# Kernel tuning notes

Measured on AMD Instinct MI355X. Metric: run time of the kernel, lower is better.

Reference implementation:

```python
import jax, jax.numpy as jnp
import numpy as np

VOCAB, EMB, HID, B, T = 50000, 16, 32, 4096, 500


def setup_inputs() -> dict:
    key = jax.random.key(0)
    k1, k2, k3, k4 = jax.random.split(key, 4)
    tokens = jax.random.randint(k1, (B, T), 0, VOCAB, dtype=jnp.int32)
    emb_table = jax.random.normal(k2, (VOCAB, EMB), dtype=jnp.float32) * 0.05
    kernel = jax.random.normal(k3, (EMB, 4 * HID), dtype=jnp.float32) * (1.0 / np.sqrt(EMB))
    rec_kernel = jax.random.normal(k4, (HID, 4 * HID), dtype=jnp.float32) * (1.0 / np.sqrt(HID))
    # Keras default: unit_forget_bias=True -> forget-gate bias = 1
    bias = jnp.concatenate([
        jnp.zeros((HID,), jnp.float32),
        jnp.ones((HID,), jnp.float32),
        jnp.zeros((2 * HID,), jnp.float32),
    ])
    return {"tokens": tokens, "emb_table": emb_table, "kernel": kernel,
            "rec_kernel": rec_kernel, "bias": bias}


def reference(tokens, emb_table, kernel, rec_kernel, bias):
    # Embedding with mask_zero=True: mask = tokens != 0
    embedded = emb_table[tokens]                 # [B, T, EMB]
    mask = (tokens != 0)                         # [B, T] bool
    # Precompute input projections for all timesteps (one big GEMM)
    x_proj = jnp.einsum('bte,eh->bth', embedded, kernel) + bias  # [B, T, 4H]

    def step(carry, xs):
        h, c = carry                              # [B, H] each
        xp_t, m_t = xs                            # [B, 4H], [B]
        z = xp_t + h @ rec_kernel                 # [B, 4H]
        i, f, g, o = jnp.split(z, 4, axis=-1)     # Keras gate order i,f,c,o
        i = jax.nn.sigmoid(i)
        f = jax.nn.sigmoid(f)
        g = jnp.tanh(g)
        o = jax.nn.sigmoid(o)
        c_new = f * c + i * g
        h_new = o * jnp.tanh(c_new)
        m = m_t[:, None]
        # masked steps carry previous state through (Keras LSTM mask semantics)
        h = jnp.where(m, h_new, h)
        c = jnp.where(m, c_new, c)
        return (h, c), None

    h0 = jnp.zeros((tokens.shape[0], HID), jnp.float32)
    c0 = jnp.zeros((tokens.shape[0], HID), jnp.float32)
    xs = (jnp.swapaxes(x_proj, 0, 1), jnp.swapaxes(mask, 0, 1))  # time-major
    (h, c), _ = jax.lax.scan(step, (h0, c0), xs)
    return h                                      # [B, HID] last (masked) output
```

## Files before the change

kernel.cpp:

```cpp
#include <hip/hip_runtime.h>
#include <cstdint>

#define VOCAB_N 50000
#define EMB_N   16
#define HID_N   32
#define B_N     4096
#define T_N     500
#define LOG2E     1.4426950408889634f
#define TWOLOG2E  2.8853900817779268f

typedef __attribute__((ext_vector_type(8))) short bf16x8;
typedef __attribute__((ext_vector_type(4))) float f32x4;
typedef __attribute__((ext_vector_type(4))) unsigned int u32x4;

__device__ __forceinline__ float frcp(float x) { return __builtin_amdgcn_rcpf(x); }

__device__ __forceinline__ unsigned bf16_split_pack(float x) {
  unsigned u  = __builtin_bit_cast(unsigned, x);
  float hif = __builtin_bit_cast(float, u & 0xFFFF0000u);
  float r   = x - hif;
  unsigned lo = __builtin_bit_cast(unsigned, r) >> 16;
  return (u >> 16) | (lo << 16);
}
__device__ __forceinline__ float unpack_h(unsigned p) {
  float hi = __builtin_bit_cast(float, p << 16);
  float lo = __builtin_bit_cast(float, p & 0xFFFF0000u);
  return hi + lo;
}

__global__ void build_proj_ns(const float* __restrict__ emb,
                              const float* __restrict__ W,
                              const float* __restrict__ bias,
                              float* __restrict__ proj) {
  __shared__ float Wl[EMB_N * 128];
  __shared__ float bl[128];
  const int tid = threadIdx.x;
  for (int i = tid; i < EMB_N * 128 / 4; i += 256)
    reinterpret_cast<float4*>(Wl)[i] = reinterpret_cast<const float4*>(W)[i];
  if (tid < 32)
    reinterpret_cast<float4*>(bl)[tid] = reinterpret_cast<const float4*>(bias)[tid];
  __syncthreads();

  const long long gid = (long long)blockIdx.x * 256 + tid;
  if (gid >= (long long)VOCAB_N * 128) return;
  const int v = (int)(gid >> 7);
  const int q = (int)(gid & 127);
  const int c  = q >> 3;
  const int par = (q >> 2) & 1;
  const int n2 = q & 3;
  const int col = (2 * n2 + par) * 16 + c;

  const float4* ev = reinterpret_cast<const float4*>(emb + (size_t)v * EMB_N);
  float4 e0 = ev[0], e1 = ev[1], e2 = ev[2], e3 = ev[3];
  const float em[16] = {e0.x,e0.y,e0.z,e0.w, e1.x,e1.y,e1.z,e1.w,
                        e2.x,e2.y,e2.z,e2.w, e3.x,e3.y,e3.z,e3.w};
  float a = bl[col];
#pragma unroll
  for (int e = 0; e < EMB_N; ++e) a = fmaf(em[e], Wl[e * 128 + col], a);
  proj[gid] = a * LOG2E;
}

#define GATE(R, TOK, CC, HH)                                                  \
  {                                                                           \
    float zi = z0[R], zf = z1[R], zg = z2[R], zo = z3[R];                     \
    float gi = frcp(1.0f + exp2f(-zi));                                       \
    float gf = frcp(1.0f + exp2f(-zf));                                       \
    float gg = fmaf(-2.0f, frcp(1.0f + exp2f(zg + zg)), 1.0f);                \
    float go = frcp(1.0f + exp2f(-zo));                                       \
    float cn = fmaf(gf, CC, gi * gg);                                         \
    float tc = fmaf(-2.0f, frcp(1.0f + exp2f(cn * TWOLOG2E)), 1.0f);          \
    float hn = go * tc;                                                       \
    bool m = (TOK) != 0;                                                      \
    CC = m ? cn : CC;                                                         \
    unsigned hp_ = bf16_split_pack(hn);                                       \
    HH = m ? hp_ : HH;                                                        \
    hl[pp ^ 1][rb + (R)][unit] = HH;                                          \
  }

#define BODY(TM, TP, X0, X1, X2, X3, TT4)                                     \
  {                                                                           \
    const unsigned* hrow = &hl[pp][c16][g8];                                  \
    u32x4 wa = *reinterpret_cast<const u32x4*>(hrow);                         \
    u32x4 wb = *reinterpret_cast<const u32x4*>(hrow + 4);                     \
    u32x4 ahp, alp;                                                           \
    ahp[0] = __builtin_amdgcn_perm(wa[1], wa[0], 0x05040100u);                \
    alp[0] = __builtin_amdgcn_perm(wa[1], wa[0], 0x07060302u);                \
    ahp[1] = __builtin_amdgcn_perm(wa[3], wa[2], 0x05040100u);                \
    alp[1] = __builtin_amdgcn_perm(wa[3], wa[2], 0x07060302u);                \
    ahp[2] = __builtin_amdgcn_perm(wb[1], wb[0], 0x05040100u);                \
    alp[2] = __builtin_amdgcn_perm(wb[1], wb[0], 0x07060302u);                \
    ahp[3] = __builtin_amdgcn_perm(wb[3], wb[2], 0x05040100u);                \
    alp[3] = __builtin_amdgcn_perm(wb[3], wb[2], 0x07060302u);                \
    bf16x8 Ah = __builtin_bit_cast(bf16x8, ahp);                              \
    bf16x8 Al = __builtin_bit_cast(bf16x8, alp);                              \
    f32x4 z0 = {(X0).x, (X1).x, (X2).x, (X3).x};                              \
    f32x4 z1 = {(X0).y, (X1).y, (X2).y, (X3).y};                              \
    f32x4 z2 = {(X0).z, (X1).z, (X2).z, (X3).z};                              \
    f32x4 z3 = {(X0).w, (X1).w, (X2).w, (X3).w};                              \
    \
    (X0) = *reinterpret_cast<const float4*>(projw + (size_t)(TP).x * 128);    \
    (X1) = *reinterpret_cast<const float4*>(projw + (size_t)(TP).y * 128);    \
    (X2) = *reinterpret_cast<const float4*>(projw + (size_t)(TP).z * 128);    \
    (X3) = *reinterpret_cast<const float4*>(projw + (size_t)(TP).w * 128);    \
    z0 = __builtin_amdgcn_mfma_f32_16x16x32_bf16(Ah, Bh0, z0, 0, 0, 0);       \
    z1 = __builtin_amdgcn_mfma_f32_16x16x32_bf16(Ah, Bh1, z1, 0, 0, 0);       \
    z2 = __builtin_amdgcn_mfma_f32_16x16x32_bf16(Ah, Bh2, z2, 0, 0, 0);       \
    z3 = __builtin_amdgcn_mfma_f32_16x16x32_bf16(Ah, Bh3, z3, 0, 0, 0);       \
    z0 = __builtin_amdgcn_mfma_f32_16x16x32_bf16(Al, Bh0, z0, 0, 0, 0);       \
    z1 = __builtin_amdgcn_mfma_f32_16x16x32_bf16(Al, Bh1, z1, 0, 0, 0);       \
    z2 = __builtin_amdgcn_mfma_f32_16x16x32_bf16(Al, Bh2, z2, 0, 0, 0);       \
    z3 = __builtin_amdgcn_mfma_f32_16x16x32_bf16(Al, Bh3, z3, 0, 0, 0);       \
    z0 = __builtin_amdgcn_mfma_f32_16x16x32_bf16(Ah, Bl0, z0, 0, 0, 0);       \
    z1 = __builtin_amdgcn_mfma_f32_16x16x32_bf16(Ah, Bl1, z1, 0, 0, 0);       \
    z2 = __builtin_amdgcn_mfma_f32_16x16x32_bf16(Ah, Bl2, z2, 0, 0, 0);       \
    z3 = __builtin_amdgcn_mfma_f32_16x16x32_bf16(Ah, Bl3, z3, 0, 0, 0);       \
                                                  \
    int4 tnew = make_int4(tokl[rb + 0][TT4], tokl[rb + 1][TT4],               \
                          tokl[rb + 2][TT4], tokl[rb + 3][TT4]);              \
    GATE(0, (TM).x, c0, hr0)                                                  \
    GATE(1, (TM).y, c1, hr1)                                                  \
    GATE(2, (TM).z, c2, hr2)                                                  \
    GATE(3, (TM).w, c3, hr3)                                                  \
    asm volatile("s_waitcnt lgkmcnt(0)" ::: "memory");                        \
    __builtin_amdgcn_s_barrier();                                             \
    asm volatile("" ::: "memory");                                            \
    __builtin_amdgcn_sched_barrier(0);                                        \
    pp ^= 1;                                                                  \
    (TM) = (TP); (TP) = tnew;                                                 \
  }

__global__ __launch_bounds__(128, 1)
void lstm_mfma_ns(const int*   __restrict__ tokens,
                  const float* __restrict__ rec_kernel,
                  const float* __restrict__ proj,
                  float*       __restrict__ out) {
  __shared__ int      tokl[16][512];
  __shared__ unsigned hl[2][16][36];

  const int tid = threadIdx.x;
  const int wv  = tid >> 6;
  const int l   = tid & 63;
  const int c16 = l & 15;
  const int g   = l >> 4;
  const int g8  = g * 8;
  const int rb  = g * 4;
  const int unit = wv * 16 + c16;

  {
    const int4* src = reinterpret_cast<const int4*>(tokens + (size_t)blockIdx.x * 16 * T_N);
    for (int i = tid; i < 16 * T_N / 4; i += 128) {
      int4 v4 = src[i];
      int gi = 4 * i;
      int r  = gi / T_N;
      int cc = gi - r * T_N;
      *reinterpret_cast<int4*>(&tokl[r][cc]) = v4;
    }
    for (int i = tid; i < 16 * 12; i += 128) {
      int r = i / 12; tokl[r][T_N + (i % 12)] = 0;
    }
  }

  hl[0][rb + 0][unit] = 0; hl[0][rb + 1][unit] = 0;
  hl[0][rb + 2][unit] = 0; hl[0][rb + 3][unit] = 0;

  bf16x8 Bh0, Bh1, Bh2, Bh3, Bl0, Bl1, Bl2, Bl3;
#define BUILD_B(Q, BH, BL)                                                    \
  {                                                                           \
    _Pragma("unroll")                                                         \
    for (int j = 0; j < 8; ++j) {                                             \
      float x = rec_kernel[(g8 + j) * 128 + (2 * (Q) + wv) * 16 + c16] * LOG2E;\
      unsigned s_ = bf16_split_pack(x);                                       \
      (BH)[j] = (short)s_; (BL)[j] = (short)(s_ >> 16);                       \
    }                                                                         \
  }
  BUILD_B(0, Bh0, Bl0) BUILD_B(1, Bh1, Bl1)
  BUILD_B(2, Bh2, Bl2) BUILD_B(3, Bh3, Bl3)
#undef BUILD_B

  __syncthreads();

  float    c0 = 0.f, c1 = 0.f, c2 = 0.f, c3 = 0.f;
  unsigned hr0 = 0, hr1 = 0, hr2 = 0, hr3 = 0;
  int pp = 0;

  int4 tmA = make_int4(tokl[rb+0][0], tokl[rb+1][0], tokl[rb+2][0], tokl[rb+3][0]);
  int4 tmB = make_int4(tokl[rb+0][1], tokl[rb+1][1], tokl[rb+2][1], tokl[rb+3][1]);
  int4 tpA = make_int4(tokl[rb+0][2], tokl[rb+1][2], tokl[rb+2][2], tokl[rb+3][2]);
  int4 tpB = make_int4(tokl[rb+0][3], tokl[rb+1][3], tokl[rb+2][3], tokl[rb+3][3]);

  const float* projw = proj + c16 * 8 + wv * 4;
  float4 xA0 = *reinterpret_cast<const float4*>(projw + (size_t)tmA.x * 128);
  float4 xA1 = *reinterpret_cast<const float4*>(projw + (size_t)tmA.y * 128);
  float4 xA2 = *reinterpret_cast<const float4*>(projw + (size_t)tmA.z * 128);
  float4 xA3 = *reinterpret_cast<const float4*>(projw + (size_t)tmA.w * 128);
  float4 xB0 = *reinterpret_cast<const float4*>(projw + (size_t)tmB.x * 128);
  float4 xB1 = *reinterpret_cast<const float4*>(projw + (size_t)tmB.y * 128);
  float4 xB2 = *reinterpret_cast<const float4*>(projw + (size_t)tmB.z * 128);
  float4 xB3 = *reinterpret_cast<const float4*>(projw + (size_t)tmB.w * 128);

#pragma unroll 1
  for (int t = 0; t < T_N; t += 2) {
    BODY(tmA, tpA, xA0, xA1, xA2, xA3, t + 4);
    BODY(tmB, tpB, xB0, xB1, xB2, xB3, t + 5);
  }

  const size_t obase = (size_t)blockIdx.x * 16 + rb;
  out[(obase + 0) * HID_N + unit] = unpack_h(hr0);
  out[(obase + 1) * HID_N + unit] = unpack_h(hr1);
  out[(obase + 2) * HID_N + unit] = unpack_h(hr2);
  out[(obase + 3) * HID_N + unit] = unpack_h(hr3);
}

__device__ __forceinline__ float sigm_fb(float x) {
  return frcp(1.0f + exp2f(x * -1.4426950408889634f));
}
__device__ __forceinline__ float tanh_fb(float x) {
  float e = exp2f(x * 2.8853900817779268f);
  return fmaf(-2.0f, frcp(e + 1.0f), 1.0f);
}

__global__ __launch_bounds__(256, 2)
void lstm_scan_fallback(const int*   __restrict__ tokens,
                        const float* __restrict__ rec_kernel,
                        const float* __restrict__ emb,
                        const float* __restrict__ W,
                        const float* __restrict__ bias,
                        float*       __restrict__ out) {
  __shared__ int   tokl[8][T_N];
  __shared__ float hbuf[8][HID_N];

  const int tid  = threadIdx.x;
  const int wv   = tid >> 6;
  const int lane = tid & 63;
  const int half = lane >> 5;
  const int j    = lane & 31;
  const int wrow = wv * 2 + half;
  const int row  = blockIdx.x * 8 + wrow;

  {
    const int4* src = reinterpret_cast<const int4*>(tokens + (size_t)blockIdx.x * 8 * T_N);
    int4* dst = reinterpret_cast<int4*>(&tokl[0][0]);
    for (int i = tid; i < 8 * T_N / 4; i += 256) dst[i] = src[i];
  }

  float wr[HID_N][4];
#pragma unroll
  for (int k = 0; k < HID_N; ++k)
#pragma unroll
    for (int gg2 = 0; gg2 < 4; ++gg2) wr[k][gg2] = rec_kernel[k * 128 + gg2 * 32 + j];

  float wk[EMB_N][4];
  float bb[4];
#pragma unroll
  for (int e = 0; e < EMB_N; ++e)
#pragma unroll
    for (int gg2 = 0; gg2 < 4; ++gg2) wk[e][gg2] = W[e * 128 + gg2 * 32 + j];
#pragma unroll
  for (int gg2 = 0; gg2 < 4; ++gg2) bb[gg2] = bias[gg2 * 32 + j];
  __syncthreads();

  float c = 0.0f, h = 0.0f;
  float4 h4[8];
#pragma unroll
  for (int q = 0; q < 8; ++q) h4[q] = make_float4(0.f, 0.f, 0.f, 0.f);

  for (int t = 0; t < T_N; ++t) {
    const int tokc = tokl[wrow][t];
    const float4* ev = reinterpret_cast<const float4*>(emb + (size_t)tokc * EMB_N);
    float4 e0 = ev[0], e1 = ev[1], e2 = ev[2], e3 = ev[3];
    const float em[16] = {e0.x,e0.y,e0.z,e0.w, e1.x,e1.y,e1.z,e1.w,
                          e2.x,e2.y,e2.z,e2.w, e3.x,e3.y,e3.z,e3.w};
    float a0 = bb[0], a1 = bb[1], a2 = bb[2], a3 = bb[3];
#pragma unroll
    for (int e = 0; e < EMB_N; ++e) {
      float x = em[e];
      a0 = fmaf(x, wk[e][0], a0); a1 = fmaf(x, wk[e][1], a1);
      a2 = fmaf(x, wk[e][2], a2); a3 = fmaf(x, wk[e][3], a3);
    }
#pragma unroll
    for (int q = 0; q < 8; ++q) {
      float hx = h4[q].x, hy = h4[q].y, hz = h4[q].z, hw = h4[q].w;
      a0 = fmaf(hx, wr[4*q+0][0], a0); a1 = fmaf(hx, wr[4*q+0][1], a1);
      a2 = fmaf(hx, wr[4*q+0][2], a2); a3 = fmaf(hx, wr[4*q+0][3], a3);
      a0 = fmaf(hy, wr[4*q+1][0], a0); a1 = fmaf(hy, wr[4*q+1][1], a1);
      a2 = fmaf(hy, wr[4*q+1][2], a2); a3 = fmaf(hy, wr[4*q+1][3], a3);
      a0 = fmaf(hz, wr[4*q+2][0], a0); a1 = fmaf(hz, wr[4*q+2][1], a1);
      a2 = fmaf(hz, wr[4*q+2][2], a2); a3 = fmaf(hz, wr[4*q+2][3], a3);
      a0 = fmaf(hw, wr[4*q+3][0], a0); a1 = fmaf(hw, wr[4*q+3][1], a1);
      a2 = fmaf(hw, wr[4*q+3][2], a2); a3 = fmaf(hw, wr[4*q+3][3], a3);
    }
    float ig = sigm_fb(a0), fg = sigm_fb(a1), gg = tanh_fb(a2), og = sigm_fb(a3);
    float cn = fmaf(fg, c, ig * gg);
    float hn = og * tanh_fb(cn);
    if (tokc != 0) { h = hn; c = cn; }
    hbuf[wrow][j] = h;
    asm volatile("" ::: "memory");
#pragma unroll
    for (int q = 0; q < 8; ++q)
      h4[q] = reinterpret_cast<const float4*>(&hbuf[wrow][0])[q];
    asm volatile("" ::: "memory");
  }
  out[(size_t)row * HID_N + j] = h;
}

extern "C" void kernel_launch(void* const* d_in, const int* in_sizes, int n_in,
                              void* d_out, int out_size, void* d_ws, size_t ws_size,
                              hipStream_t stream) {
  const int*   tokens = (const int*)  d_in[0];
  const float* emb    = (const float*)d_in[1];
  const float* W      = (const float*)d_in[2];
  const float* rec    = (const float*)d_in[3];
  const float* bias   = (const float*)d_in[4];
  float* out = (float*)d_out;

  const size_t need = (size_t)VOCAB_N * 128 * sizeof(float);
  if (ws_size >= need) {
    float* proj = (float*)d_ws;
    const long long total = (long long)VOCAB_N * 128;
    build_proj_ns<<<(int)((total + 255) / 256), 256, 0, stream>>>(emb, W, bias, proj);
    lstm_mfma_ns<<<B_N / 16, 128, 0, stream>>>(tokens, rec, proj, out);
  } else {
    lstm_scan_fallback<<<B_N / 8, 256, 0, stream>>>(tokens, rec, emb, W, bias, out);
  }
}
```

Before: 392.9 us.

## Transpose LSTM recurrence into single-wave MFMA with register-resident hidden state

The recurrent matmul is rewritten as W^T·h^T, so one 64-lane wave per 16-row batch tile holds all 128 gate columns. The hidden state stays in registers, packed as the MFMA B operand, which removes the per-step LDS round trip and the two-wave barrier. The projection table is permuted to match the new output layout, and the tanh-gate columns are prescaled by 2·log2e so the gate math saves a multiply. In exchange each wave issues 24 MFMAs per step with only 64 threads per block, which lowers occupancy and latency hiding.

After: 709.8 us. 1.81x slower.

```diff
diff --git a/kernel.cpp b/kernel.cpp
--- a/kernel.cpp
+++ b/kernel.cpp
@@ -28,10 +28,19 @@
   return hi + lo;
 }
 
-__global__ void build_proj_ns(const float* __restrict__ emb,
-                              const float* __restrict__ W,
-                              const float* __restrict__ bias,
-                              float* __restrict__ proj) {
+__device__ __forceinline__ int map_col(int p) {
+  int n = p >> 4, s = p & 15;
+  int g = s >> 2, r = s & 3;
+  return 32 * (n >> 1) + 8 * g + 2 * r + (n & 1);
+}
+__device__ __forceinline__ float col_scale(int n) {
+  return (n == 4 || n == 5) ? TWOLOG2E : LOG2E;
+}
+
+__global__ void build_proj_t(const float* __restrict__ emb,
+                             const float* __restrict__ W,
+                             const float* __restrict__ bias,
+                             float* __restrict__ proj) {
   __shared__ float Wl[EMB_N * 128];
   __shared__ float bl[128];
   const int tid = threadIdx.x;
@@ -44,11 +53,9 @@
   const long long gid = (long long)blockIdx.x * 256 + tid;
   if (gid >= (long long)VOCAB_N * 128) return;
   const int v = (int)(gid >> 7);
-  const int q = (int)(gid & 127);
-  const int c  = q >> 3;
-  const int par = (q >> 2) & 1;
-  const int n2 = q & 3;
-  const int col = (2 * n2 + par) * 16 + c;
+  const int p = (int)(gid & 127);
+  const int col = map_col(p);
+  const float sc = col_scale(p >> 4);
 
   const float4* ev = reinterpret_cast<const float4*>(emb + (size_t)v * EMB_N);
   float4 e0 = ev[0], e1 = ev[1], e2 = ev[2], e3 = ev[3];
@@ -57,158 +64,176 @@
   float a = bl[col];
 #pragma unroll
   for (int e = 0; e < EMB_N; ++e) a = fmaf(em[e], Wl[e * 128 + col], a);
-  proj[gid] = a * LOG2E;
-}
-
-#define GATE(R, TOK, CC, HH)                                                  \
+  proj[gid] = a * sc;
+}
+
+#define MF(A_, B_, C_) __builtin_amdgcn_mfma_f32_16x16x32_bf16((A_), (B_), (C_), 0, 0, 0)
+
+#define GATE(HP, CC, ZI, ZF, ZG, ZO, R)                                       \
   {                                                                           \
-    float zi = z0[R], zf = z1[R], zg = z2[R], zo = z3[R];                     \
+    float zi = (ZI)[R], zf = (ZF)[R], zg = (ZG)[R], zo = (ZO)[R];             \
     float gi = frcp(1.0f + exp2f(-zi));                                       \
     float gf = frcp(1.0f + exp2f(-zf));                                       \
-    float gg = fmaf(-2.0f, frcp(1.0f + exp2f(zg + zg)), 1.0f);                \
+    float gg = fmaf(-2.0f, frcp(1.0f + exp2f(zg)), 1.0f);                     \
     float go = frcp(1.0f + exp2f(-zo));                                       \
-    float cn = fmaf(gf, CC, gi * gg);                                         \
+    float cn = fmaf(gf, (CC), gi * gg);                                       \
     float tc = fmaf(-2.0f, frcp(1.0f + exp2f(cn * TWOLOG2E)), 1.0f);          \
     float hn = go * tc;                                                       \
-    bool m = (TOK) != 0;                                                      \
-    CC = m ? cn : CC;                                                         \
+    (CC) = mk ? cn : (CC);                                                    \
     unsigned hp_ = bf16_split_pack(hn);                                       \
-    HH = m ? hp_ : HH;                                                        \
-    hl[pp ^ 1][rb + (R)][unit] = HH;                                          \
-  }
-
-#define BODY(TM, TP, X0, X1, X2, X3, TT4)                                     \
+    (HP) = mk ? hp_ : (HP);                                                   \
+  }
+
+#define MBODY(TKC, TKP, XX0, XX1, XX2, XX3, XX4, XX5, XX6, XX7)               \
   {                                                                           \
-    const unsigned* hrow = &hl[pp][c16][g8];                                  \
-    u32x4 wa = *reinterpret_cast<const u32x4*>(hrow);                         \
-    u32x4 wb = *reinterpret_cast<const u32x4*>(hrow + 4);                     \
-    u32x4 ahp, alp;                                                           \
-    ahp[0] = __builtin_amdgcn_perm(wa[1], wa[0], 0x05040100u);                \
-    alp[0] = __builtin_amdgcn_perm(wa[1], wa[0], 0x07060302u);                \
-    ahp[1] = __builtin_amdgcn_perm(wa[3], wa[2], 0x05040100u);                \
-    alp[1] = __builtin_amdgcn_perm(wa[3], wa[2], 0x07060302u);                \
-    ahp[2] = __builtin_amdgcn_perm(wb[1], wb[0], 0x05040100u);                \
-    alp[2] = __builtin_amdgcn_perm(wb[1], wb[0], 0x07060302u);                \
-    ahp[3] = __builtin_amdgcn_perm(wb[3], wb[2], 0x05040100u);                \
-    alp[3] = __builtin_amdgcn_perm(wb[3], wb[2], 0x07060302u);                \
-    bf16x8 Ah = __builtin_bit_cast(bf16x8, ahp);                              \
-    bf16x8 Al = __builtin_bit_cast(bf16x8, alp);                              \
-    f32x4 z0 = {(X0).x, (X1).x, (X2).x, (X3).x};                              \
-    f32x4 z1 = {(X0).y, (X1).y, (X2).y, (X3).y};                              \
-    f32x4 z2 = {(X0).z, (X1).z, (X2).z, (X3).z};                              \
-    f32x4 z3 = {(X0).w, (X1).w, (X2).w, (X3).w};                              \
-    \
-    (X0) = *reinterpret_cast<const float4*>(projw + (size_t)(TP).x * 128);    \
-    (X1) = *reinterpret_cast<const float4*>(projw + (size_t)(TP).y * 128);    \
-    (X2) = *reinterpret_cast<const float4*>(projw + (size_t)(TP).z * 128);    \
-    (X3) = *reinterpret_cast<const float4*>(projw + (size_t)(TP).w * 128);    \
-    z0 = __builtin_amdgcn_mfma_f32_16x16x32_bf16(Ah, Bh0, z0, 0, 0, 0);       \
-    z1 = __builtin_amdgcn_mfma_f32_16x16x32_bf16(Ah, Bh1, z1, 0, 0, 0);       \
-    z2 = __builtin_amdgcn_mfma_f32_16x16x32_bf16(Ah, Bh2, z2, 0, 0, 0);       \
-    z3 = __builtin_amdgcn_mfma_f32_16x16x32_bf16(Ah, Bh3, z3, 0, 0, 0);       \
-    z0 = __builtin_amdgcn_mfma_f32_16x16x32_bf16(Al, Bh0, z0, 0, 0, 0);       \
-    z1 = __builtin_amdgcn_mfma_f32_16x16x32_bf16(Al, Bh1, z1, 0, 0, 0);       \
-    z2 = __builtin_amdgcn_mfma_f32_16x16x32_bf16(Al, Bh2, z2, 0, 0, 0);       \
-    z3 = __builtin_amdgcn_mfma_f32_16x16x32_bf16(Al, Bh3, z3, 0, 0, 0);       \
-    z0 = __builtin_amdgcn_mfma_f32_16x16x32_bf16(Ah, Bl0, z0, 0, 0, 0);       \
-    z1 = __builtin_amdgcn_mfma_f32_16x16x32_bf16(Ah, Bl1, z1, 0, 0, 0);       \
-    z2 = __builtin_amdgcn_mfma_f32_16x16x32_bf16(Ah, Bl2, z2, 0, 0, 0);       \
-    z3 = __builtin_amdgcn_mfma_f32_16x16x32_bf16(Ah, Bl3, z3, 0, 0, 0);       \
-                                                  \
-    int4 tnew = make_int4(tokl[rb + 0][TT4], tokl[rb + 1][TT4],               \
-                          tokl[rb + 2][TT4], tokl[rb + 3][TT4]);              \
-    GATE(0, (TM).x, c0, hr0)                                                  \
-    GATE(1, (TM).y, c1, hr1)                                                  \
-    GATE(2, (TM).z, c2, hr2)                                                  \
-    GATE(3, (TM).w, c3, hr3)                                                  \
-    asm volatile("s_waitcnt lgkmcnt(0)" ::: "memory");                        \
-    __builtin_amdgcn_s_barrier();                                             \
-    asm volatile("" ::: "memory");                                            \
-    __builtin_amdgcn_sched_barrier(0);                                        \
-    pp ^= 1;                                                                  \
-    (TM) = (TP); (TP) = tnew;                                                 \
-  }
-
-__global__ __launch_bounds__(128, 1)
-void lstm_mfma_ns(const int*   __restrict__ tokens,
-                  const float* __restrict__ rec_kernel,
-                  const float* __restrict__ proj,
-                  float*       __restrict__ out) {
-  __shared__ int      tokl[16][512];
-  __shared__ unsigned hl[2][16][36];
-
-  const int tid = threadIdx.x;
-  const int wv  = tid >> 6;
-  const int l   = tid & 63;
+                  \
+    u32x4 bhv, blv;                                                           \
+    bhv[0] = __builtin_amdgcn_perm(hp1, hp0, 0x05040100u);                    \
+    blv[0] = __builtin_amdgcn_perm(hp1, hp0, 0x07060302u);                    \
+    bhv[1] = __builtin_amdgcn_perm(hp3, hp2, 0x05040100u);                    \
+    blv[1] = __builtin_amdgcn_perm(hp3, hp2, 0x07060302u);                    \
+    bhv[2] = __builtin_amdgcn_perm(hp5, hp4, 0x05040100u);                    \
+    blv[2] = __builtin_amdgcn_perm(hp5, hp4, 0x07060302u);                    \
+    bhv[3] = __builtin_amdgcn_perm(hp7, hp6, 0x05040100u);                    \
+    blv[3] = __builtin_amdgcn_perm(hp7, hp6, 0x07060302u);                    \
+    bf16x8 Bh = __builtin_bit_cast(bf16x8, bhv);                              \
+    bf16x8 Bl = __builtin_bit_cast(bf16x8, blv);                              \
+    f32x4 za0 = __builtin_bit_cast(f32x4, XX0);                               \
+    f32x4 za1 = __builtin_bit_cast(f32x4, XX1);                               \
+    f32x4 za2 = __builtin_bit_cast(f32x4, XX2);                               \
+    f32x4 za3 = __builtin_bit_cast(f32x4, XX3);                               \
+    f32x4 za4 = __builtin_bit_cast(f32x4, XX4);                               \
+    f32x4 za5 = __builtin_bit_cast(f32x4, XX5);                               \
+    f32x4 za6 = __builtin_bit_cast(f32x4, XX6);                               \
+    f32x4 za7 = __builtin_bit_cast(f32x4, XX7);                               \
+                                     \
+    za0 = MF(Ah0, Bh, za0); za0 = MF(Ah0, Bl, za0); za0 = MF(Al0, Bh, za0);   \
+    za2 = MF(Ah2, Bh, za2); za2 = MF(Ah2, Bl, za2); za2 = MF(Al2, Bh, za2);   \
+    za4 = MF(Ah4, Bh, za4); za4 = MF(Ah4, Bl, za4); za4 = MF(Al4, Bh, za4);   \
+    za6 = MF(Ah6, Bh, za6); za6 = MF(Ah6, Bl, za6); za6 = MF(Al6, Bh, za6);   \
+                              \
+    {                                                                         \
+      const float* pv = proj + ((size_t)(unsigned)(TKP) << 7) + g4;           \
+      XX0 = *reinterpret_cast<const float4*>(pv);                             \
+      XX1 = *reinterpret_cast<const float4*>(pv + 16);                        \
+      XX2 = *reinterpret_cast<const float4*>(pv + 32);                        \
+      XX3 = *reinterpret_cast<const float4*>(pv + 48);                        \
+      XX4 = *reinterpret_cast<const float4*>(pv + 64);                        \
+      XX5 = *reinterpret_cast<const float4*>(pv + 80);                        \
+      XX6 = *reinterpret_cast<const float4*>(pv + 96);                        \
+      XX7 = *reinterpret_cast<const float4*>(pv + 112);                       \
+    }                                                                         \
+    const bool mk = (TKC) != 0;                                               \
+    GATE(hp0, cc0, za0, za2, za4, za6, 0)                                     \
+    GATE(hp2, cc2, za0, za2, za4, za6, 1)                                     \
+    GATE(hp4, cc4, za0, za2, za4, za6, 2)                                     \
+    GATE(hp6, cc6, za0, za2, za4, za6, 3)                                     \
+    za1 = MF(Ah1, Bh, za1); za1 = MF(Ah1, Bl, za1); za1 = MF(Al1, Bh, za1);   \
+    za3 = MF(Ah3, Bh, za3); za3 = MF(Ah3, Bl, za3); za3 = MF(Al3, Bh, za3);   \
+    za5 = MF(Ah5, Bh, za5); za5 = MF(Ah5, Bl, za5); za5 = MF(Al5, Bh, za5);   \
+    za7 = MF(Ah7, Bh, za7); za7 = MF(Ah7, Bl, za7); za7 = MF(Al7, Bh, za7);   \
+    GATE(hp1, cc1, za1, za3, za5, za7, 0)                                     \
+    GATE(hp3, cc3, za1, za3, za5, za7, 1)                                     \
+    GATE(hp5, cc5, za1, za3, za5, za7, 2)                                     \
+    GATE(hp7, cc7, za1, za3, za5, za7, 3)                                     \
+  }
+
+__global__ __launch_bounds__(64, 1)
+void lstm_mfma_t(const int*   __restrict__ tokens,
+                 const float* __restrict__ rec_kernel,
+                 const float* __restrict__ proj,
+                 float*       __restrict__ out) {
+  __shared__ int tokl[16][516];
+
+  const int l   = threadIdx.x;
+  const int g   = l >> 4;
   const int c16 = l & 15;
-  const int g   = l >> 4;
   const int g8  = g * 8;
-  const int rb  = g * 4;
-  const int unit = wv * 16 + c16;
+  const int g4  = g * 4;
 
   {
     const int4* src = reinterpret_cast<const int4*>(tokens + (size_t)blockIdx.x * 16 * T_N);
-    for (int i = tid; i < 16 * T_N / 4; i += 128) {
+    for (int i = l; i < 16 * T_N / 4; i += 64) {
       int4 v4 = src[i];
       int gi = 4 * i;
       int r  = gi / T_N;
       int cc = gi - r * T_N;
       *reinterpret_cast<int4*>(&tokl[r][cc]) = v4;
     }
-    for (int i = tid; i < 16 * 12; i += 128) {
-      int r = i / 12; tokl[r][T_N + (i % 12)] = 0;
+    for (int i = l; i < 16 * 16; i += 64) {
+      int r = i >> 4; tokl[r][T_N + (i & 15)] = 0;
     }
   }
 
-  hl[0][rb + 0][unit] = 0; hl[0][rb + 1][unit] = 0;
-  hl[0][rb + 2][unit] = 0; hl[0][rb + 3][unit] = 0;
-
-  bf16x8 Bh0, Bh1, Bh2, Bh3, Bl0, Bl1, Bl2, Bl3;
-#define BUILD_B(Q, BH, BL)                                                    \
+  bf16x8 Ah0, Ah1, Ah2, Ah3, Ah4, Ah5, Ah6, Ah7;
+  bf16x8 Al0, Al1, Al2, Al3, Al4, Al5, Al6, Al7;
+#define BUILD_A(N, AH, AL)                                                    \
   {                                                                           \
+    const int Cn = map_col(16 * (N) + c16);                                   \
+    const float sc = col_scale(N);                                            \
     _Pragma("unroll")                                                         \
     for (int j = 0; j < 8; ++j) {                                             \
-      float x = rec_kernel[(g8 + j) * 128 + (2 * (Q) + wv) * 16 + c16] * LOG2E;\
+      float x = rec_kernel[(g8 + j) * 128 + Cn] * sc;                         \
       unsigned s_ = bf16_split_pack(x);                                       \
-      (BH)[j] = (short)s_; (BL)[j] = (short)(s_ >> 16);                       \
+      (AH)[j] = (short)s_; (AL)[j] = (short)(s_ >> 16);                       \
     }                                                                         \
   }
-  BUILD_B(0, Bh0, Bl0) BUILD_B(1, Bh1, Bl1)
-  BUILD_B(2, Bh2, Bl2) BUILD_B(3, Bh3, Bl3)
-#undef BUILD_B
-
-  __syncthreads();
-
-  float    c0 = 0.f, c1 = 0.f, c2 = 0.f, c3 = 0.f;
-  unsigned hr0 = 0, hr1 = 0, hr2 = 0, hr3 = 0;
-  int pp = 0;
-
-  int4 tmA = make_int4(tokl[rb+0][0], tokl[rb+1][0], tokl[rb+2][0], tokl[rb+3][0]);
-  int4 tmB = make_int4(tokl[rb+0][1], tokl[rb+1][1], tokl[rb+2][1], tokl[rb+3][1]);
-  int4 tpA = make_int4(tokl[rb+0][2], tokl[rb+1][2], tokl[rb+2][2], tokl[rb+3][2]);
-  int4 tpB = make_int4(tokl[rb+0][3], tokl[rb+1][3], tokl[rb+2][3], tokl[rb+3][3]);
-
-  const float* projw = proj + c16 * 8 + wv * 4;
-  float4 xA0 = *reinterpret_cast<const float4*>(projw + (size_t)tmA.x * 128);
-  float4 xA1 = *reinterpret_cast<const float4*>(projw + (size_t)tmA.y * 128);
-  float4 xA2 = *reinterpret_cast<const float4*>(projw + (size_t)tmA.z * 128);
-  float4 xA3 = *reinterpret_cast<const float4*>(projw + (size_t)tmA.w * 128);
-  float4 xB0 = *reinterpret_cast<const float4*>(projw + (size_t)tmB.x * 128);
-  float4 xB1 = *reinterpret_cast<const float4*>(projw + (size_t)tmB.y * 128);
-  float4 xB2 = *reinterpret_cast<const float4*>(projw + (size_t)tmB.z * 128);
-  float4 xB3 = *reinterpret_cast<const float4*>(projw + (size_t)tmB.w * 128);
+  BUILD_A(0, Ah0, Al0) BUILD_A(1, Ah1, Al1) BUILD_A(2, Ah2, Al2)
+  BUILD_A(3, Ah3, Al3) BUILD_A(4, Ah4, Al4) BUILD_A(5, Ah5, Al5)
+  BUILD_A(6, Ah6, Al6) BUILD_A(7, Ah7, Al7)
+#undef BUILD_A
+
+  asm volatile("s_waitcnt lgkmcnt(0)" ::: "memory");
+
+  unsigned hp0 = 0, hp1 = 0, hp2 = 0, hp3 = 0, hp4 = 0, hp5 = 0, hp6 = 0, hp7 = 0;
+  float    cc0 = 0.f, cc1 = 0.f, cc2 = 0.f, cc3 = 0.f,
+           cc4 = 0.f, cc5 = 0.f, cc6 = 0.f, cc7 = 0.f;
+
+  int tk0 = tokl[c16][0];
+  int tk1 = tokl[c16][1];
+  int tk2 = tokl[c16][2];
+  int tk3 = tokl[c16][3];
+
+  float4 XA0, XA1, XA2, XA3, XA4, XA5, XA6, XA7;
+  float4 XB0, XB1, XB2, XB3, XB4, XB5, XB6, XB7;
+  {
+    const float* pv = proj + ((size_t)(unsigned)tk0 << 7) + g4;
+    XA0 = *reinterpret_cast<const float4*>(pv);
+    XA1 = *reinterpret_cast<const float4*>(pv + 16);
+    XA2 = *reinterpret_cast<const float4*>(pv + 32);
+    XA3 = *reinterpret_cast<const float4*>(pv + 48);
+    XA4 = *reinterpret_cast<const float4*>(pv + 64);
+    XA5 = *reinterpret_cast<const float4*>(pv + 80);
+    XA6 = *reinterpret_cast<const float4*>(pv + 96);
+    XA7 = *reinterpret_cast<const float4*>(pv + 112);
+    const float* pw = proj + ((size_t)(unsigned)tk1 << 7) + g4;
+    XB0 = *reinterpret_cast<const float4*>(pw);
+    XB1 = *reinterpret_cast<const float4*>(pw + 16);
+    XB2 = *reinterpret_cast<const float4*>(pw + 32);
+    XB3 = *reinterpret_cast<const float4*>(pw + 48);
+    XB4 = *reinterpret_cast<const float4*>(pw + 64);
+    XB5 = *reinterpret_cast<const float4*>(pw + 80);
+    XB6 = *reinterpret_cast<const float4*>(pw + 96);
+    XB7 = *reinterpret_cast<const float4*>(pw + 112);
+  }
 
 #pragma unroll 1
   for (int t = 0; t < T_N; t += 2) {
-    BODY(tmA, tpA, xA0, xA1, xA2, xA3, t + 4);
-    BODY(tmB, tpB, xB0, xB1, xB2, xB3, t + 5);
-  }
-
-  const size_t obase = (size_t)blockIdx.x * 16 + rb;
-  out[(obase + 0) * HID_N + unit] = unpack_h(hr0);
-  out[(obase + 1) * HID_N + unit] = unpack_h(hr1);
-  out[(obase + 2) * HID_N + unit] = unpack_h(hr2);
-  out[(obase + 3) * HID_N + unit] = unpack_h(hr3);
+    int tn0 = tokl[c16][t + 4];
+    int tn1 = tokl[c16][t + 5];
+
+    MBODY(tk0, tk2, XA0, XA1, XA2, XA3, XA4, XA5, XA6, XA7);
+    MBODY(tk1, tk3, XB0, XB1, XB2, XB3, XB4, XB5, XB6, XB7);
+
+    tk0 = tk2; tk1 = tk3; tk2 = tn0; tk3 = tn1;
+  }
+
+  float4 o0, o1;
+  o0.x = unpack_h(hp0); o0.y = unpack_h(hp1); o0.z = unpack_h(hp2); o0.w = unpack_h(hp3);
+  o1.x = unpack_h(hp4); o1.y = unpack_h(hp5); o1.z = unpack_h(hp6); o1.w = unpack_h(hp7);
+  float* ob = out + ((size_t)blockIdx.x * 16 + c16) * HID_N + g8;
+  *reinterpret_cast<float4*>(ob)     = o0;
+  *reinterpret_cast<float4*>(ob + 4) = o1;
 }
 
 __device__ __forceinline__ float sigm_fb(float x) {
@@ -317,8 +342,8 @@
   if (ws_size >= need) {
     float* proj = (float*)d_ws;
     const long long total = (long long)VOCAB_N * 128;
-    build_proj_ns<<<(int)((total + 255) / 256), 256, 0, stream>>>(emb, W, bias, proj);
-    lstm_mfma_ns<<<B_N / 16, 128, 0, stream>>>(tokens, rec, proj, out);
+    build_proj_t<<<(int)((total + 255) / 256), 256, 0, stream>>>(emb, W, bias, proj);
+    lstm_mfma_t<<<B_N / 16, 64, 0, stream>>>(tokens, rec, proj, out);
   } else {
     lstm_scan_fallback<<<B_N / 8, 256, 0, stream>>>(tokens, rec, emb, W, bias, out);
   }
```
